# Performance work log

Measured on AMD Instinct MI355X. Metric: run time of the kernel, lower is better.

## Reference

```python
import jax, jax.numpy as jnp
import numpy as np


def setup_inputs() -> dict:
    key = jax.random.key(0)
    k1, k2, k3, k4 = jax.random.split(key, 4)
    B, N, F_in, F_out = 8, 2048, 256, 128
    h = jax.random.normal(k1, (B, N, F_in), dtype=jnp.float32)
    # fc: Linear(in_features, out_features, bias=False); store as [F_in, F_out]
    W_fc = jax.random.normal(k2, (F_in, F_out), dtype=jnp.float32) * (1.0 / np.sqrt(F_in))
    # attn_fc: Linear(2*F_out, 1, bias=False) -> split into the two additive halves
    a_i = jax.random.normal(k3, (F_out,), dtype=jnp.float32) * (1.0 / np.sqrt(2 * F_out))
    a_j = jax.random.normal(k4, (F_out,), dtype=jnp.float32) * (1.0 / np.sqrt(2 * F_out))
    return {"h": h, "W_fc": W_fc, "a_i": a_i, "a_j": a_j}


def reference(h, W_fc, a_i, a_j):
    # Wh: [B, N, F_out]
    Wh = jnp.einsum("bnf,fo->bno", h, W_fc)
    # attn_fc(cat([Wh_i, Wh_j])) is linear, so it decomposes additively:
    # e[b,i,j] = <Wh[b,i], a_i> + <Wh[b,j], a_j>  -- same math, no N^2*2F tensor
    s_i = Wh @ a_i  # [B, N]
    s_j = Wh @ a_j  # [B, N]
    e = s_i[:, :, None] + s_j[:, None, :]  # [B, N, N]
    alpha = jax.nn.softmax(jax.nn.leaky_relu(e, negative_slope=0.01), axis=-1)
    h_prime = jnp.einsum("bij,bjo->bio", alpha, Wh)  # [B, N, F_out]
    return h_prime
```

## Files before the change

### kernel.cpp

```cpp
#include <hip/hip_runtime.h>
#include <hip/hip_bf16.h>

#define BATCH 8
#define NN 2048
#define FIN 256
#define FOUT 128
#define ROWS (BATCH*NN)
#define NP1 (NN+1)
#define SEGS 128
#define SLEN (NN/SEGS)

typedef __attribute__((ext_vector_type(8))) __bf16 bf16x8;
typedef __attribute__((ext_vector_type(4))) float f32x4;
typedef __attribute__((ext_vector_type(8))) unsigned short ushort8_t;

__device__ __forceinline__ unsigned pack2(float a, float b){
  __hip_bfloat16 x = __float2bfloat16(a), y = __float2bfloat16(b);
  unsigned short ux = *(unsigned short*)&x, uy = *(unsigned short*)&y;
  return ((unsigned)uy << 16) | (unsigned)ux;
}
__device__ __forceinline__ float lo2f(unsigned u){ union{unsigned v;float f;}c; c.v = u << 16; return c.f; }
__device__ __forceinline__ float hi2f(unsigned u){ union{unsigned v;float f;}c; c.v = u & 0xffff0000u; return c.f; }

__device__ __forceinline__ void bsplit(float x, unsigned short& hu, unsigned short& lu){
  __hip_bfloat16 hb = __float2bfloat16(x);
  hu = *(unsigned short*)&hb;
  union{unsigned u; float f;} hf; hf.u = (unsigned)hu << 16;
  __hip_bfloat16 lb = __float2bfloat16(x - hf.f);
  lu = *(unsigned short*)&lb;
}

__global__ __launch_bounds__(256) void k_wsplit(const float* __restrict__ W,
                                                unsigned short* __restrict__ Wth,
                                                unsigned short* __restrict__ Wtl){
  const int gid = blockIdx.x * 256 + threadIdx.x;
  const int k = gid >> 5, c4 = (gid & 31) * 4;
  float4 v = *(const float4*)&W[(size_t)k * FOUT + c4];
  float xs[4] = {v.x, v.y, v.z, v.w};
  #pragma unroll
  for (int i = 0; i < 4; i++){
    unsigned short hu, lu;
    bsplit(xs[i], hu, lu);
    Wth[(size_t)(c4 + i) * FIN + k] = hu;
    Wtl[(size_t)(c4 + i) * FIN + k] = lu;
  }
}

__global__ __launch_bounds__(256) void k_gemm(const float* __restrict__ h,
                                              const unsigned short* __restrict__ Wth,
                                              const unsigned short* __restrict__ Wtl,
                                              const float* __restrict__ ai,
                                              const float* __restrict__ aj,
                                              float* __restrict__ Wh,
                                              float* __restrict__ sI,
                                              float* __restrict__ sJ){
  __shared__ unsigned short Ah[32*40], Al[32*40];
  __shared__ unsigned short Bh[128*40], Bl[128*40];
  __shared__ float spI[2][32], spJ[2][32];
  const int t = threadIdx.x;
  const int rbase = blockIdx.x * 32;
  const int b = rbase >> 11;
  const int brow0 = rbase & (NN - 1);
  const int w = t >> 6, l = t & 63;
  const int g = w & 1, cg = w >> 1;
  const int lr = l & 15, lq = l >> 4;
  const int sar = t >> 3, sak = (t & 7) * 4;
  const int sbc = t >> 1, sbh = (t & 1) * 16;

  f32x4 acc[4];
  #pragma unroll
  for (int ct = 0; ct < 4; ct++) acc[ct] = (f32x4){0.f, 0.f, 0.f, 0.f};

  for (int k0 = 0; k0 < FIN; k0 += 32){
    {
      float4 hv = *(const float4*)&h[(size_t)(rbase + sar) * FIN + k0 + sak];
      float xs[4] = {hv.x, hv.y, hv.z, hv.w};
      ushort4 hh, ll;
      unsigned short hu, lu;
      bsplit(xs[0], hu, lu); hh.x = hu; ll.x = lu;
      bsplit(xs[1], hu, lu); hh.y = hu; ll.y = lu;
      bsplit(xs[2], hu, lu); hh.z = hu; ll.z = lu;
      bsplit(xs[3], hu, lu); hh.w = hu; ll.w = lu;
      *(ushort4*)&Ah[sar * 40 + sak] = hh;
      *(ushort4*)&Al[sar * 40 + sak] = ll;
    }
    {
      const size_t gb = (size_t)sbc * FIN + k0 + sbh;
      ushort8_t b0 = *(const ushort8_t*)&Wth[gb];
      ushort8_t b1 = *(const ushort8_t*)&Wth[gb + 8];
      ushort8_t c0 = *(const ushort8_t*)&Wtl[gb];
      ushort8_t c1 = *(const ushort8_t*)&Wtl[gb + 8];
      *(ushort8_t*)&Bh[sbc * 40 + sbh]     = b0;
      *(ushort8_t*)&Bh[sbc * 40 + sbh + 8] = b1;
      *(ushort8_t*)&Bl[sbc * 40 + sbh]     = c0;
      *(ushort8_t*)&Bl[sbc * 40 + sbh + 8] = c1;
    }
    __syncthreads();
    const bf16x8 avh = __builtin_bit_cast(bf16x8, *(const ushort8_t*)&Ah[(g*16 + lr)*40 + lq*8]);
    const bf16x8 avl = __builtin_bit_cast(bf16x8, *(const ushort8_t*)&Al[(g*16 + lr)*40 + lq*8]);
    #pragma unroll
    for (int ct = 0; ct < 4; ct++){
      const int col = cg*64 + ct*16 + lr;
      const bf16x8 bvh = __builtin_bit_cast(bf16x8, *(const ushort8_t*)&Bh[col*40 + lq*8]);
      const bf16x8 bvl = __builtin_bit_cast(bf16x8, *(const ushort8_t*)&Bl[col*40 + lq*8]);
      acc[ct] = __builtin_amdgcn_mfma_f32_16x16x32_bf16(avh, bvh, acc[ct], 0, 0, 0);
      acc[ct] = __builtin_amdgcn_mfma_f32_16x16x32_bf16(avh, bvl, acc[ct], 0, 0, 0);
      acc[ct] = __builtin_amdgcn_mfma_f32_16x16x32_bf16(avl, bvh, acc[ct], 0, 0, 0);
    }
    __syncthreads();
  }
  float pi[4] = {0.f,0.f,0.f,0.f}, pj[4] = {0.f,0.f,0.f,0.f};
  #pragma unroll
  for (int ct = 0; ct < 4; ct++){
    const int col = cg*64 + ct*16 + lr;
    const int og = col >> 2, ol2 = col & 3;
    const float fai = ai[col], faj = aj[col];
    const size_t obase = ((size_t)(b * 32 + og) * NN + brow0 + g*16 + lq*4) * 4 + ol2;
    #pragma unroll
    for (int q = 0; q < 4; q++){
      const float val = acc[ct][q];
      Wh[obase + (size_t)q * 4] = val;
      pi[q] = fmaf(val, fai, pi[q]);
      pj[q] = fmaf(val, faj, pj[q]);
    }
  }
  #pragma unroll
  for (int q = 0; q < 4; q++){
    #pragma unroll
    for (int m = 1; m < 16; m <<= 1){
      pi[q] += __shfl_xor(pi[q], m);
      pj[q] += __shfl_xor(pj[q], m);
    }
  }
  if (lr == 0){
    #pragma unroll
    for (int q = 0; q < 4; q++){
      spI[cg][g*16 + lq*4 + q] = pi[q];
      spJ[cg][g*16 + lq*4 + q] = pj[q];
    }
  }
  __syncthreads();
  if (t < 32){
    sI[rbase + t] = spI[0][t] + spI[1][t];
    sJ[rbase + t] = spJ[0][t] + spJ[1][t];
  }
}

__global__ __launch_bounds__(256) void k_rank_scatter(const float* __restrict__ sJ,
                                                      float* __restrict__ sortedS,
                                                      int* __restrict__ perm,
                                                      float2* __restrict__ e12g){
  const int b = blockIdx.x >> 6;
  const int jc = blockIdx.x & 63;
  __shared__ float v[NN];
  __shared__ int partial[8][32];
  const int t = threadIdx.x;
  const float* sj = sJ + b * NN;
  #pragma unroll
  for (int u = 0; u < 2; u++)
    ((float4*)v)[t + u * 256] = ((const float4*)sj)[t + u * 256];
  const int jj = t & 31, qq = t >> 5;
  const int j = jc * 32 + jj;
  const float x = sj[j];
  __syncthreads();
  const int q0 = qq * 256;
  int r = 0;
  #pragma unroll 8
  for (int q4 = 0; q4 < 64; q4++){
    const int q = q0 + q4 * 4;
    float4 y = *(const float4*)&v[q];
    r += (y.x < x) || (y.x == x && (q + 0) < j);
    r += (y.y < x) || (y.y == x && (q + 1) < j);
    r += (y.z < x) || (y.z == x && (q + 2) < j);
    r += (y.w < x) || (y.w == x && (q + 3) < j);
  }
  partial[qq][jj] = r;
  __syncthreads();
  if (t < 32){
    int R = 0;
    #pragma unroll
    for (int q8 = 0; q8 < 8; q8++) R += partial[q8][t];
    const int myj = jc * 32 + t;
    const float xx = v[myj];
    sortedS[b * NN + R] = xx;
    perm[b * NN + R] = myj;
    e12g[b * NN + R] = make_float2(expf(xx), expf(0.01f * xx));
  }
}

__global__ __launch_bounds__(512) void k_fuseout(const float* __restrict__ sortedS,
                                                 const float* __restrict__ sI,
                                                 const float2* __restrict__ e12g,
                                                 const float* __restrict__ Wh,
                                                 const int* __restrict__ perm,
                                                 float* __restrict__ out){
  __shared__ float    ssL[NN];
  __shared__ float2   abL[NP1];
  __shared__ unsigned PL[NP1][4];
  __shared__ float wtP1[8][4], wtP2[8][4], wtS1[8], wtS2[8];
  const int bc = blockIdx.x;
  const int b = bc >> 5;
  const int og = bc & 31;
  const int t = threadIdx.x;
  const int ol = t & 3;
  const int seg = t >> 2;
  const int r0 = seg * SLEN;
  const int wv = t >> 6, wl = t & 63;

  const float* ssg = sortedS + b * NN;
  #pragma unroll
  for (int u = 0; u < 4; u++) ssL[t + u * 512] = ssg[t + u * 512];

  const int*    pm  = perm + b * NN;
  const float2* e12 = e12g + b * NN;
  const float*  whb = Wh + (size_t)(b * 32 + og) * NN * 4;
  float w[SLEN], ex[SLEN], ey[SLEN];
  float t1 = 0.f, t2 = 0.f, s1 = 0.f, s2 = 0.f;
  #pragma unroll
  for (int r = 0; r < SLEN; r++){
    w[r] = whb[(size_t)pm[r0 + r] * 4 + ol];
    const float2 u = e12[r0 + r];
    ex[r] = u.x; ey[r] = u.y;
    t1 = fmaf(u.x, w[r], t1);
    t2 = fmaf(u.y, w[r], t2);
    s1 += u.x; s2 += u.y;
  }
  float c1 = t1, c2 = t2, cs1 = s1, cs2 = s2;
  #pragma unroll
  for (int d = 1; d < 16; d <<= 1){
    const float u1 = __shfl_up(c1, d * 4);
    const float u2 = __shfl_up(c2, d * 4);
    const float u3 = __shfl_up(cs1, d * 4);
    const float u4 = __shfl_up(cs2, d * 4);
    if ((wl >> 2) >= d){ c1 += u1; c2 += u2; cs1 += u3; cs2 += u4; }
  }
  if ((wl >> 2) == 15){
    wtP1[wv][ol] = c1; wtP2[wv][ol] = c2;
    if (ol == 0){ wtS1[wv] = cs1; wtS2[wv] = cs2; }
  }
  __syncthreads();
  for (int ww = 0; ww < wv; ww++){
    c1 += wtP1[ww][ol]; c2 += wtP2[ww][ol];
    cs1 += wtS1[ww];    cs2 += wtS2[ww];
  }
  float acc1 = c1 - t1;
  float acc2 = c2 - t2;
  if (seg == 0){
    PL[0][ol] = 0u;
    if (ol == 0) abL[0] = make_float2(0.f, 0.f);
  }
  {
    float offs1 = 0.f, offs2 = 0.f;
    if (ol == 0){ offs1 = cs1 - s1; offs2 = cs2 - s2; }
    float run1 = 0.f, run2 = 0.f;
    #pragma unroll
    for (int r = 0; r < SLEN; r++){
      acc1 = fmaf(ex[r], w[r], acc1);
      acc2 = fmaf(ey[r], w[r], acc2);
      PL[r0 + r + 1][ol] = pack2(acc1, acc2);
      if (ol == 0){
        run1 += ex[r]; run2 += ey[r];
        abL[r0 + r + 1] = make_float2(offs1 + run1, offs2 + run2);
      }
    }
  }
  __syncthreads();
  const int tg = t >> 2;
  float sv[16];
  #pragma unroll
  for (int u = 0; u < 16; u++) sv[u] = sI[b * NN + tg + u * 128];
  int lo[16], hi[16];
  #pragma unroll
  for (int u = 0; u < 16; u++){ lo[u] = 0; hi[u] = NN; }
  #pragma unroll
  for (int step = 0; step < 11; step++){
    float mv[16]; int mid[16];
    #pragma unroll
    for (int u = 0; u < 16; u++){
      mid[u] = (lo[u] + hi[u]) >> 1;
      mv[u] = ssL[mid[u]];
    }
    #pragma unroll
    for (int u = 0; u < 16; u++){
      if (mv[u] <= -sv[u]) lo[u] = mid[u] + 1; else hi[u] = mid[u];
    }
  }
  const float2 vT = abL[NN];
  const unsigned uTp = PL[NN][ol];
  #pragma unroll
  for (int u = 0; u < 16; u++){
    const int row = tg + u * 128;
    const int k = lo[u];
    const float s = sv[u];
    const float w1 = expf(s), w2 = expf(0.01f * s);
    const float2 vk = abL[k];
    const float inv = 1.0f / (w1 * (vT.x - vk.x) + w2 * vk.y);
    const unsigned uk = PL[k][ol];
    const float num = w1 * (lo2f(uTp) - lo2f(uk)) + w2 * hi2f(uk);
    out[(size_t)(b * NN + row) * FOUT + og * 4 + ol] = num * inv;
  }
}

extern "C" void kernel_launch(void* const* d_in, const int* in_sizes, int n_in,
                              void* d_out, int out_size, void* d_ws, size_t ws_size,
                              hipStream_t stream){
  const float* h  = (const float*)d_in[0];
  const float* W  = (const float*)d_in[1];
  const float* ai = (const float*)d_in[2];
  const float* aj = (const float*)d_in[3];
  float* out = (float*)d_out;

  char* ws = (char*)d_ws;
  size_t off = 0;
  auto alloc = [&](size_t bytes) -> void* {
    void* p = ws + off;
    off += (bytes + 255) & ~(size_t)255;
    return p;
  };
  float*          Wh   = (float*)   alloc((size_t)ROWS * FOUT * 4);
  float*          sI   = (float*)   alloc((size_t)ROWS * 4);
  float*          sJ   = (float*)   alloc((size_t)ROWS * 4);
  float*          sortedS = (float*)alloc((size_t)BATCH * NN * 4);
  int*            perm = (int*)     alloc((size_t)BATCH * NN * 4);
  float2*         e12  = (float2*)  alloc((size_t)BATCH * NN * 8);
  unsigned short* Wth  = (unsigned short*)alloc((size_t)FOUT * FIN * 2);
  unsigned short* Wtl  = (unsigned short*)alloc((size_t)FOUT * FIN * 2);

  k_wsplit      <<<32, 256, 0, stream>>>(W, Wth, Wtl);
  k_gemm        <<<ROWS / 32, 256, 0, stream>>>(h, Wth, Wtl, ai, aj, Wh, sI, sJ);
  k_rank_scatter<<<BATCH * 64, 256, 0, stream>>>(sJ, sortedS, perm, e12);
  k_fuseout     <<<BATCH * 32, 512, 0, stream>>>(sortedS, sI, e12, Wh, perm, out);
}
```

Before: 109.8 us.

## Compute split index in rank kernel and pack permuted exp/perm into float4

The split point for each row (count of sJ values <= -sI) is now computed by brute-force counting in the rank-scatter kernel, alongside the rank. This removes the per-block binary search over a shared sorted array in the output kernel, which was repeated by all 32 column-group blocks per batch. The permuted exp values and permutation index are packed into one float4 so each gather needs a single load. The trade-off is extra compare work in the rank kernel and wider per-element stores.

```diff
diff --git a/kernel.cpp b/kernel.cpp
--- a/kernel.cpp
+++ b/kernel.cpp
@@ -147,13 +147,14 @@
 }
 
 __global__ __launch_bounds__(256) void k_rank_scatter(const float* __restrict__ sJ,
-                                                      float* __restrict__ sortedS,
-                                                      int* __restrict__ perm,
-                                                      float2* __restrict__ e12g){
+                                                      const float* __restrict__ sI,
+                                                      float4* __restrict__ pe4,
+                                                      float2* __restrict__ skP){
   const int b = blockIdx.x >> 6;
   const int jc = blockIdx.x & 63;
   __shared__ float v[NN];
-  __shared__ int partial[8][32];
+  __shared__ int partialR[8][32];
+  __shared__ int partialC[8][32];
   const int t = threadIdx.x;
   const float* sj = sJ + b * NN;
   #pragma unroll
@@ -162,9 +163,10 @@
   const int jj = t & 31, qq = t >> 5;
   const int j = jc * 32 + jj;
   const float x = sj[j];
+  const float key = -sI[b * NN + j];
   __syncthreads();
   const int q0 = qq * 256;
-  int r = 0;
+  int r = 0, c = 0;
   #pragma unroll 8
   for (int q4 = 0; q4 < 64; q4++){
     const int q = q0 + q4 * 4;
@@ -173,28 +175,29 @@
     r += (y.y < x) || (y.y == x && (q + 1) < j);
     r += (y.z < x) || (y.z == x && (q + 2) < j);
     r += (y.w < x) || (y.w == x && (q + 3) < j);
-  }
-  partial[qq][jj] = r;
+    c += (y.x <= key);
+    c += (y.y <= key);
+    c += (y.z <= key);
+    c += (y.w <= key);
+  }
+  partialR[qq][jj] = r;
+  partialC[qq][jj] = c;
   __syncthreads();
   if (t < 32){
-    int R = 0;
-    #pragma unroll
-    for (int q8 = 0; q8 < 8; q8++) R += partial[q8][t];
+    int R = 0, C = 0;
+    #pragma unroll
+    for (int q8 = 0; q8 < 8; q8++){ R += partialR[q8][t]; C += partialC[q8][t]; }
     const int myj = jc * 32 + t;
     const float xx = v[myj];
-    sortedS[b * NN + R] = xx;
-    perm[b * NN + R] = myj;
-    e12g[b * NN + R] = make_float2(expf(xx), expf(0.01f * xx));
-  }
-}
-
-__global__ __launch_bounds__(512) void k_fuseout(const float* __restrict__ sortedS,
-                                                 const float* __restrict__ sI,
-                                                 const float2* __restrict__ e12g,
+    pe4[b * NN + R] = make_float4(expf(xx), expf(0.01f * xx), __int_as_float(myj), 0.f);
+    skP[b * NN + myj] = make_float2(sI[b * NN + myj], __int_as_float(C));
+  }
+}
+
+__global__ __launch_bounds__(512) void k_fuseout(const float2* __restrict__ skP,
+                                                 const float4* __restrict__ pe4,
                                                  const float* __restrict__ Wh,
-                                                 const int* __restrict__ perm,
                                                  float* __restrict__ out){
-  __shared__ float    ssL[NN];
   __shared__ float2   abL[NP1];
   __shared__ unsigned PL[NP1][4];
   __shared__ float wtP1[8][4], wtP2[8][4], wtS1[8], wtS2[8];
@@ -207,19 +210,15 @@
   const int r0 = seg * SLEN;
   const int wv = t >> 6, wl = t & 63;
 
-  const float* ssg = sortedS + b * NN;
-  #pragma unroll
-  for (int u = 0; u < 4; u++) ssL[t + u * 512] = ssg[t + u * 512];
-
-  const int*    pm  = perm + b * NN;
-  const float2* e12 = e12g + b * NN;
+  const float4* pe  = pe4 + b * NN;
   const float*  whb = Wh + (size_t)(b * 32 + og) * NN * 4;
   float w[SLEN], ex[SLEN], ey[SLEN];
   float t1 = 0.f, t2 = 0.f, s1 = 0.f, s2 = 0.f;
   #pragma unroll
   for (int r = 0; r < SLEN; r++){
-    w[r] = whb[(size_t)pm[r0 + r] * 4 + ol];
-    const float2 u = e12[r0 + r];
+    const float4 u = pe[r0 + r];
+    const int pmr = __float_as_int(u.z);
+    w[r] = whb[(size_t)pmr * 4 + ol];
     ex[r] = u.x; ey[r] = u.y;
     t1 = fmaf(u.x, w[r], t1);
     t2 = fmaf(u.y, w[r], t2);
@@ -266,32 +265,15 @@
   }
   __syncthreads();
   const int tg = t >> 2;
-  float sv[16];
-  #pragma unroll
-  for (int u = 0; u < 16; u++) sv[u] = sI[b * NN + tg + u * 128];
-  int lo[16], hi[16];
-  #pragma unroll
-  for (int u = 0; u < 16; u++){ lo[u] = 0; hi[u] = NN; }
-  #pragma unroll
-  for (int step = 0; step < 11; step++){
-    float mv[16]; int mid[16];
-    #pragma unroll
-    for (int u = 0; u < 16; u++){
-      mid[u] = (lo[u] + hi[u]) >> 1;
-      mv[u] = ssL[mid[u]];
-    }
-    #pragma unroll
-    for (int u = 0; u < 16; u++){
-      if (mv[u] <= -sv[u]) lo[u] = mid[u] + 1; else hi[u] = mid[u];
-    }
-  }
+  const float2* skb = skP + b * NN;
   const float2 vT = abL[NN];
   const unsigned uTp = PL[NN][ol];
   #pragma unroll
   for (int u = 0; u < 16; u++){
     const int row = tg + u * 128;
-    const int k = lo[u];
-    const float s = sv[u];
+    const float2 sk = skb[row];
+    const float s = sk.x;
+    const int k = __float_as_int(sk.y);
     const float w1 = expf(s), w2 = expf(0.01f * s);
     const float2 vk = abL[k];
     const float inv = 1.0f / (w1 * (vT.x - vk.x) + w2 * vk.y);
@@ -320,14 +302,13 @@
   float*          Wh   = (float*)   alloc((size_t)ROWS * FOUT * 4);
   float*          sI   = (float*)   alloc((size_t)ROWS * 4);
   float*          sJ   = (float*)   alloc((size_t)ROWS * 4);
-  float*          sortedS = (float*)alloc((size_t)BATCH * NN * 4);
-  int*            perm = (int*)     alloc((size_t)BATCH * NN * 4);
-  float2*         e12  = (float2*)  alloc((size_t)BATCH * NN * 8);
+  float4*         pe4  = (float4*)  alloc((size_t)BATCH * NN * 16);
+  float2*         skP  = (float2*)  alloc((size_t)BATCH * NN * 8);
   unsigned short* Wth  = (unsigned short*)alloc((size_t)FOUT * FIN * 2);
   unsigned short* Wtl  = (unsigned short*)alloc((size_t)FOUT * FIN * 2);
 
   k_wsplit      <<<32, 256, 0, stream>>>(W, Wth, Wtl);
   k_gemm        <<<ROWS / 32, 256, 0, stream>>>(h, Wth, Wtl, ai, aj, Wh, sI, sJ);
-  k_rank_scatter<<<BATCH * 64, 256, 0, stream>>>(sJ, sortedS, perm, e12);
-  k_fuseout     <<<BATCH * 32, 512, 0, stream>>>(sortedS, sI, e12, Wh, perm, out);
-}
+  k_rank_scatter<<<BATCH * 64, 256, 0, stream>>>(sJ, sI, pe4, skP);
+  k_fuseout     <<<BATCH * 32, 512, 0, stream>>>(skP, pe4, Wh, out);
+}
```

After: 107.1 us. -2.4%, faster.
